# Kernel optimization log

Measured on AMD Instinct MI355X. Metric: run time of the kernel, lower is better.

The kernel has to match this reference:

```python
import jax, jax.numpy as jnp
import numpy as np

CUTOFF = 5.0
NUM_RADIAL = 6
HIDDEN = 128
N_NODES = 100000
N_EDGES = 800000
MAX_Z = 95
P = 6  # envelope_exponent(5) + 1, per PyG Envelope


def _envelope(x):
    # PyG DimeNet Envelope: (1/x + a*x^(p-1) + b*x^p + c*x^(p+1)) * (x < 1)
    a = -(P + 1) * (P + 2) / 2.0   # -28
    b = P * (P + 2)                # 48
    c = -P * (P + 1) / 2.0         # -21
    xp0 = x ** (P - 1)
    xp1 = xp0 * x
    xp2 = xp1 * x
    return (1.0 / x + a * xp0 + b * xp1 + c * xp2) * (x < 1.0)


def setup_inputs():
    key = jax.random.key(0)
    ks = jax.random.split(key, 8)
    z = jax.random.randint(ks[0], (N_NODES,), 0, MAX_Z, dtype=jnp.int32)
    pos = jax.random.normal(ks[1], (N_NODES, 3), dtype=jnp.float32)
    ei = jax.random.randint(ks[2], (2, N_EDGES), 0, N_NODES, dtype=jnp.int32)
    i, j = ei[0], ei[1]
    j = jnp.where(j == i, (j + 1) % N_NODES, j)  # radius_graph emits no self-loops (avoids d=0)
    edge_index = jnp.stack([i, j])
    # BesselBasisLayer learnable frequencies: pi * n
    freq = np.pi * jnp.arange(1, NUM_RADIAL + 1, dtype=jnp.float32)
    s3 = float(np.sqrt(3.0))
    emb_table = jax.random.uniform(ks[3], (MAX_Z, HIDDEN), jnp.float32, -s3, s3)
    W_rbf = jax.random.normal(ks[4], (NUM_RADIAL, HIDDEN), jnp.float32) * (1.0 / np.sqrt(NUM_RADIAL))
    b_rbf = jnp.zeros((HIDDEN,), jnp.float32)
    W_lin = jax.random.normal(ks[5], (3 * HIDDEN, HIDDEN), jnp.float32) * (1.0 / np.sqrt(3 * HIDDEN))
    b_lin = jnp.zeros((HIDDEN,), jnp.float32)
    return {"z": z, "pos": pos, "edge_index": edge_index, "freq": freq,
            "emb_table": emb_table, "W_rbf": W_rbf, "b_rbf": b_rbf,
            "W_lin": W_lin, "b_lin": b_lin}


def reference(z, pos, edge_index, freq, emb_table, W_rbf, b_rbf, W_lin, b_lin):
    n = z.shape[0]
    i, j = edge_index[0], edge_index[1]
    # per-edge distance  [E]
    d = jnp.sqrt(jnp.sum((pos[i] - pos[j]) ** 2, axis=-1))
    # Bessel RBF  [E, num_radial]
    x = d[:, None] / CUTOFF
    rbf = _envelope(x) * jnp.sin(freq * x)
    # DimeNet EmbeddingBlock (act = SiLU/swish)
    h_rbf = jax.nn.silu(rbf @ W_rbf + b_rbf)            # [E, H]
    xz = emb_table[z]                                    # [N, H]
    e_emb = jax.nn.silu(
        jnp.concatenate([xz[i], xz[j], h_rbf], axis=-1) @ W_lin + b_lin
    )                                                    # [E, H]
    # scatter_mean over target node j -> [N, H]
    sums = jax.ops.segment_sum(e_emb, j, num_segments=n)
    cnt = jax.ops.segment_sum(jnp.ones_like(d), j, num_segments=n)
    v_emb = sums / jnp.maximum(cnt, 1.0)[:, None]
    return v_emb  # pool=None -> node-level embeddings
```

## Files before the change

### kernel.cpp

```cpp
#include <hip/hip_runtime.h>
#include <hip/hip_bf16.h>
#include <math.h>

#define HID 128
#define NRAD 6
#define TABN 4096
#define CUTOFF_INV 0.2f
#define MZ 95
#define MZP (MZ + 1)
#define SENT ((MZ << 13) | (MZ << 20))
#define PAD 32
#define OVF_CAP 65536
#define FTR 8

typedef unsigned int uint32;

__global__ void build1(const float* __restrict__ emb, const float* __restrict__ W_lin,
                       const float* __restrict__ freq, const float* __restrict__ W_rbf,
                       const float* __restrict__ b_rbf, const float* __restrict__ b_lin,
                       const int* __restrict__ ei, const float* __restrict__ pos,
                       const int* __restrict__ z,
                       __hip_bfloat16* __restrict__ Tb, float* __restrict__ ftab,
                       int* __restrict__ cnt, int* __restrict__ payload,
                       int* __restrict__ ovfcnt, int2* __restrict__ ovfbuf,
                       int MAXZ, int E) {
    __shared__ float sh[FTR * HID];
    int h   = threadIdx.x;
    int bid = blockIdx.x;
    int nT  = 2 * (MAXZ + 1);
    int nF  = (TABN + FTR) / FTR;
    if (bid < nT) {
        int zz = bid >> 1, s = bid & 1;
        if (zz == MAXZ) {
            Tb[(size_t)(s * (MAXZ + 1) + zz) * HID + h] = __float2bfloat16(-60.0f);
            return;
        }
        sh[h] = emb[zz * HID + h];
        __syncthreads();
        const float* W = W_lin + (size_t)s * HID * HID;
        float acc = (s == 0) ? b_lin[h] : 0.f;
#pragma unroll 8
        for (int k = 0; k < HID; ++k) acc = fmaf(sh[k], W[k * HID + h], acc);
        Tb[(size_t)(s * (MAXZ + 1) + zz) * HID + h] = __float2bfloat16(acc);
    } else if (bid < nT + nF) {
        int t0 = (bid - nT) * FTR;
        for (int r = 0; r < FTR; ++r) {
            int t = t0 + r;
            float rbf[NRAD];
            if (t == 0) {
#pragma unroll
                for (int k = 0; k < NRAD; ++k) rbf[k] = freq[k];
            } else if (t >= TABN) {
#pragma unroll
                for (int k = 0; k < NRAD; ++k) rbf[k] = 0.f;
            } else {
                float x  = (float)t / (float)TABN;
                float x2 = x * x, x5 = x2 * x2 * x;
                float env = 1.f / x + x5 * (-28.f + x * (48.f + x * (-21.f)));
#pragma unroll
                for (int k = 0; k < NRAD; ++k) rbf[k] = env * sinf(freq[k] * x);
            }
            float pre = b_rbf[h];
#pragma unroll
            for (int k = 0; k < NRAD; ++k) pre = fmaf(rbf[k], W_rbf[k * HID + h], pre);
            sh[r * HID + h] = pre / (1.f + __expf(-pre));
        }
        __syncthreads();
        const float* W3 = W_lin + (size_t)2 * HID * HID;
        float acc[FTR];
#pragma unroll
        for (int r = 0; r < FTR; ++r) acc[r] = 0.f;
#pragma unroll 4
        for (int k = 0; k < HID; ++k) {
            float w = W3[k * HID + h];
#pragma unroll
            for (int r = 0; r < FTR; ++r) acc[r] = fmaf(sh[r * HID + k], w, acc[r]);
        }
        for (int r = 0; r < FTR; ++r) {
            int t = t0 + r;
            if (t <= TABN) ftab[(size_t)t * HID + h] = acc[r];
        }
    } else {
        int e = (bid - nT - nF) * HID + h;
        if (e < E) {
            int i = ei[e];
            int j = ei[E + e];
            float dx = pos[3 * i]     - pos[3 * j];
            float dy = pos[3 * i + 1] - pos[3 * j + 1];
            float dz = pos[3 * i + 2] - pos[3 * j + 2];
            float d  = sqrtf(dx * dx + dy * dy + dz * dz);
            float u  = fminf(d * CUTOFF_INV, 1.0f) * (float)TABN;
            int   ti = (int)(u + 0.5f);
            if (ti > TABN) ti = TABN;
            int pl = ti | (z[i] << 13) | (z[j] << 20);
            int r  = atomicAdd(&cnt[j], 1);
            if (r < PAD) {
                payload[(size_t)j * PAD + r] = pl;
            } else {
                int o = atomicAdd(ovfcnt, 1);
                if (o < OVF_CAP) ovfbuf[o] = make_int2(j, pl);
            }
        }
    }
}

#define EDGE_ACC(pl_) do {                                                                    \
    int ti_ = (pl_) & 0x1FFF;                                                                 \
    int zi_ = ((pl_) >> 13) & 0x7F;                                                           \
    int zj_ = ((pl_) >> 20) & 0x7F;                                                           \
    float4 f_ = *(const float4*)((const char*)ftab + (uint32)((ti_ << 9) + fb4));             \
    uint32 a0_ = sT[zi_ * (HID / 2) + l2];                                                    \
    uint32 a1_ = sT[zi_ * (HID / 2) + l2 + 1];                                                \
    uint32 b0_ = sT[(MZP + zj_) * (HID / 2) + l2];                                            \
    uint32 b1_ = sT[(MZP + zj_) * (HID / 2) + l2 + 1];                                        \
    float p0_ = __uint_as_float(a0_ << 16)         + __uint_as_float(b0_ << 16)         + f_.x; \
    float p1_ = __uint_as_float(a0_ & 0xFFFF0000u) + __uint_as_float(b0_ & 0xFFFF0000u) + f_.y; \
    float p2_ = __uint_as_float(a1_ << 16)         + __uint_as_float(b1_ << 16)         + f_.z; \
    float p3_ = __uint_as_float(a1_ & 0xFFFF0000u) + __uint_as_float(b1_ & 0xFFFF0000u) + f_.w; \
    ax = fmaf(p0_, __builtin_amdgcn_rcpf(1.f + __expf(-p0_)), ax);                            \
    ay = fmaf(p1_, __builtin_amdgcn_rcpf(1.f + __expf(-p1_)), ay);                            \
    az = fmaf(p2_, __builtin_amdgcn_rcpf(1.f + __expf(-p2_)), az);                            \
    aw = fmaf(p3_, __builtin_amdgcn_rcpf(1.f + __expf(-p3_)), aw);                            \
} while (0)

__launch_bounds__(1024)
__global__ void gather_k(const int* __restrict__ cnt, const int* __restrict__ payload,
                         const uint32* __restrict__ Tb32, const float* __restrict__ ftab,
                         const int* __restrict__ ovfcnt, const int2* __restrict__ ovfbuf,
                         float* __restrict__ out, int N) {
    __shared__ uint32 sT[2 * MZP * (HID / 2)];
    int tid = threadIdx.x;
    for (int k = tid; k < 2 * MZP * (HID / 2); k += 1024) sT[k] = Tb32[k];
    __syncthreads();

    int lane = tid & 63, wv = tid >> 6;
    int hi   = lane >> 5;
    int l32  = lane & 31;
    int h4   = l32 * 4;
    int l2   = l32 * 2;
    uint32 fb4 = (uint32)h4 << 2;
    int nov  = *ovfcnt;
    if (nov > OVF_CAP) nov = OVF_CAP;
    int nW = gridDim.x << 4;

    for (int n = (blockIdx.x << 4) + wv; n < N; n += nW) {
        int deg = cnt[n];
        int plv = payload[(size_t)n * PAD + l32];
        int cb  = deg < PAD ? deg : PAD;
        plv = (l32 < cb) ? plv : SENT;
        int nit = (cb + 1) >> 1;

        float ax = 0.f, ay = 0.f, az = 0.f, aw = 0.f;
        for (int k = 0; k < nit; ++k) {
            int plA = __builtin_amdgcn_readlane(plv, 2 * k);
            int plB = __builtin_amdgcn_readlane(plv, 2 * k + 1);
            int pl  = hi ? plB : plA;
            EDGE_ACC(pl);
        }
        if (deg > PAD && nov > 0) {
            for (int o = 0; o < nov; ++o) {
                int2 v = ovfbuf[o];
                if (v.x == n) { int pl = v.y; EDGE_ACC(pl); }
            }
        }
        ax += __shfl_xor(ax, 32);
        ay += __shfl_xor(ay, 32);
        az += __shfl_xor(az, 32);
        aw += __shfl_xor(aw, 32);
        if (hi == 0) {
            float s = (deg > 0) ? 1.0f / (float)deg : 0.0f;
            float4 o4;
            o4.x = ax * s; o4.y = ay * s; o4.z = az * s; o4.w = aw * s;
            *(float4*)(out + (size_t)n * HID + h4) = o4;
        }
    }
}

extern "C" void kernel_launch(void* const* d_in, const int* in_sizes, int n_in,
                              void* d_out, int out_size, void* d_ws, size_t ws_size,
                              hipStream_t stream) {
    const int*   z     = (const int*)d_in[0];
    const float* pos   = (const float*)d_in[1];
    const int*   ei    = (const int*)d_in[2];
    const float* freq  = (const float*)d_in[3];
    const float* emb   = (const float*)d_in[4];
    const float* W_rbf = (const float*)d_in[5];
    const float* b_rbf = (const float*)d_in[6];
    const float* W_lin = (const float*)d_in[7];
    const float* b_lin = (const float*)d_in[8];

    int N    = in_sizes[0];
    int E    = in_sizes[2] / 2;
    int MAXZ = in_sizes[4] / HID;
    float* out = (float*)d_out;

    int N_pad = ((N + 1024) / 1024) * 1024;

    char* ws = (char*)d_ws;
    size_t off = 0;
    auto alloc = [&](size_t bytes) { char* p = ws + off; off = (off + bytes + 255) & ~(size_t)255; return p; };
    int*   cnt     = (int*)alloc((size_t)N_pad * 4);
    int*   ovfcnt  = (int*)alloc(256);
    __hip_bfloat16* Tb = (__hip_bfloat16*)alloc((size_t)2 * (MAXZ + 1) * HID * 2);
    float* ftab    = (float*)alloc((size_t)(TABN + 1) * HID * 4);
    int*   payload = (int*)alloc((size_t)N_pad * PAD * 4);
    int2*  ovfbuf  = (int2*)alloc((size_t)OVF_CAP * 8);

    hipMemsetAsync(cnt, 0, (size_t)N_pad * 4 + 256, stream);

    int nBuild = 2 * (MAXZ + 1) + (TABN + FTR) / FTR + (E + HID - 1) / HID;
    build1<<<nBuild, HID, 0, stream>>>(emb, W_lin, freq, W_rbf, b_rbf, b_lin,
                                       ei, pos, z, Tb, ftab, cnt, payload,
                                       ovfcnt, ovfbuf, MAXZ, E);
    gather_k<<<512, 1024, 0, stream>>>(cnt, payload, (const uint32*)Tb, ftab,
                                       ovfcnt, ovfbuf, out, N);
}
```

Baseline: 186.8 us.

## Software-pipeline gather loop, prefetch next node, and fold log2e into tables

The gather loop is software-pipelined: the ftab float4 load for the edge two ahead and the LDS table loads for the next edge are issued before the current edge's compute. Node degree and payload for the next node are prefetched across iterations. The tables are prescaled by log2(e) so the SiLU uses a raw v_exp_f32 with a negated operand, and the result is rescaled by ln2 at output. The sentinel value changes to keep the padded-edge contribution near zero in the new scaling. LDS reads are also widened to uint2. This adds register pressure and relies on the wrapped readlane index hitting sentinel lanes for the tail.

Result: no change. 188.3 us (+0.8%).

```diff
diff --git a/kernel.cpp b/kernel.cpp
--- a/kernel.cpp
+++ b/kernel.cpp
@@ -12,6 +12,8 @@
 #define PAD 32
 #define OVF_CAP 65536
 #define FTR 8
+#define LOG2E 1.4426950408889634f
+#define LN2   0.6931471805599453f
 
 typedef unsigned int uint32;
 
@@ -32,7 +34,7 @@
     if (bid < nT) {
         int zz = bid >> 1, s = bid & 1;
         if (zz == MAXZ) {
-            Tb[(size_t)(s * (MAXZ + 1) + zz) * HID + h] = __float2bfloat16(-60.0f);
+            Tb[(size_t)(s * (MAXZ + 1) + zz) * HID + h] = __float2bfloat16(-86.5f);
             return;
         }
         sh[h] = emb[zz * HID + h];
@@ -41,7 +43,7 @@
         float acc = (s == 0) ? b_lin[h] : 0.f;
 #pragma unroll 8
         for (int k = 0; k < HID; ++k) acc = fmaf(sh[k], W[k * HID + h], acc);
-        Tb[(size_t)(s * (MAXZ + 1) + zz) * HID + h] = __float2bfloat16(acc);
+        Tb[(size_t)(s * (MAXZ + 1) + zz) * HID + h] = __float2bfloat16(acc * LOG2E);
     } else if (bid < nT + nF) {
         int t0 = (bid - nT) * FTR;
         for (int r = 0; r < FTR; ++r) {
@@ -78,7 +80,7 @@
         }
         for (int r = 0; r < FTR; ++r) {
             int t = t0 + r;
-            if (t <= TABN) ftab[(size_t)t * HID + h] = acc[r];
+            if (t <= TABN) ftab[(size_t)t * HID + h] = acc[r] * LOG2E;
         }
     } else {
         int e = (bid - nT - nF) * HID + h;
@@ -104,23 +106,31 @@
     }
 }
 
-#define EDGE_ACC(pl_) do {                                                                    \
-    int ti_ = (pl_) & 0x1FFF;                                                                 \
-    int zi_ = ((pl_) >> 13) & 0x7F;                                                           \
-    int zj_ = ((pl_) >> 20) & 0x7F;                                                           \
-    float4 f_ = *(const float4*)((const char*)ftab + (uint32)((ti_ << 9) + fb4));             \
-    uint32 a0_ = sT[zi_ * (HID / 2) + l2];                                                    \
-    uint32 a1_ = sT[zi_ * (HID / 2) + l2 + 1];                                                \
-    uint32 b0_ = sT[(MZP + zj_) * (HID / 2) + l2];                                            \
-    uint32 b1_ = sT[(MZP + zj_) * (HID / 2) + l2 + 1];                                        \
-    float p0_ = __uint_as_float(a0_ << 16)         + __uint_as_float(b0_ << 16)         + f_.x; \
-    float p1_ = __uint_as_float(a0_ & 0xFFFF0000u) + __uint_as_float(b0_ & 0xFFFF0000u) + f_.y; \
-    float p2_ = __uint_as_float(a1_ << 16)         + __uint_as_float(b1_ << 16)         + f_.z; \
-    float p3_ = __uint_as_float(a1_ & 0xFFFF0000u) + __uint_as_float(b1_ & 0xFFFF0000u) + f_.w; \
-    ax = fmaf(p0_, __builtin_amdgcn_rcpf(1.f + __expf(-p0_)), ax);                            \
-    ay = fmaf(p1_, __builtin_amdgcn_rcpf(1.f + __expf(-p1_)), ay);                            \
-    az = fmaf(p2_, __builtin_amdgcn_rcpf(1.f + __expf(-p2_)), az);                            \
-    aw = fmaf(p3_, __builtin_amdgcn_rcpf(1.f + __expf(-p3_)), aw);                            \
+__device__ __forceinline__ float exp2neg(float x) {
+    float r; asm("v_exp_f32 %0, -%1" : "=v"(r) : "v"(x)); return r;
+}
+
+#define PLSEL(pv_, idx_) (hi ? __builtin_amdgcn_readlane((pv_), 2 * (idx_) + 1) \
+                             : __builtin_amdgcn_readlane((pv_), 2 * (idx_)))
+
+#define FLOAD(pl_) (*(const float4*)((const char*)ftab + (uint32)((((pl_) & 0x1FFF) << 9) + fb4)))
+
+#define TL(pl_, ua_, ub_) do {                                                 \
+    int zi_ = ((pl_) >> 13) & 0x7F;                                            \
+    int zj_ = ((pl_) >> 20) & 0x7F;                                            \
+    ua_ = *(const uint2*)&sT[zi_ * (HID / 2) + l2];                            \
+    ub_ = *(const uint2*)&sT[(MZP + zj_) * (HID / 2) + l2];                    \
+} while (0)
+
+#define COMPUTE(f_, ua_, ub_) do {                                                                 \
+    float p0_ = __uint_as_float(ua_.x << 16)         + __uint_as_float(ub_.x << 16)         + f_.x; \
+    float p1_ = __uint_as_float(ua_.x & 0xFFFF0000u) + __uint_as_float(ub_.x & 0xFFFF0000u) + f_.y; \
+    float p2_ = __uint_as_float(ua_.y << 16)         + __uint_as_float(ub_.y << 16)         + f_.z; \
+    float p3_ = __uint_as_float(ua_.y & 0xFFFF0000u) + __uint_as_float(ub_.y & 0xFFFF0000u) + f_.w; \
+    ax = fmaf(p0_, __builtin_amdgcn_rcpf(1.f + exp2neg(p0_)), ax);                                 \
+    ay = fmaf(p1_, __builtin_amdgcn_rcpf(1.f + exp2neg(p1_)), ay);                                 \
+    az = fmaf(p2_, __builtin_amdgcn_rcpf(1.f + exp2neg(p2_)), az);                                 \
+    aw = fmaf(p3_, __builtin_amdgcn_rcpf(1.f + exp2neg(p3_)), aw);                                 \
 } while (0)
 
 __launch_bounds__(1024)
@@ -138,29 +148,53 @@
     int l32  = lane & 31;
     int h4   = l32 * 4;
     int l2   = l32 * 2;
-    uint32 fb4 = (uint32)h4 << 2;
+    uint32 fb4 = (uint32)l32 << 4;
     int nov  = *ovfcnt;
     if (nov > OVF_CAP) nov = OVF_CAP;
     int nW = gridDim.x << 4;
 
-    for (int n = (blockIdx.x << 4) + wv; n < N; n += nW) {
-        int deg = cnt[n];
-        int plv = payload[(size_t)n * PAD + l32];
+    int n = (blockIdx.x << 4) + wv;
+    int degC = 0, plvC = SENT;
+    if (n < N) { degC = cnt[n]; plvC = payload[(size_t)n * PAD + l32]; }
+
+    while (n < N) {
+        int n2 = n + nW;
+        int degN = 0, plvN = SENT;
+        if (n2 < N) { degN = cnt[n2]; plvN = payload[(size_t)n2 * PAD + l32]; }
+
+        int deg = degC;
         int cb  = deg < PAD ? deg : PAD;
-        plv = (l32 < cb) ? plv : SENT;
+        int plv = (l32 < cb) ? plvC : SENT;
         int nit = (cb + 1) >> 1;
 
         float ax = 0.f, ay = 0.f, az = 0.f, aw = 0.f;
-        for (int k = 0; k < nit; ++k) {
-            int plA = __builtin_amdgcn_readlane(plv, 2 * k);
-            int plB = __builtin_amdgcn_readlane(plv, 2 * k + 1);
-            int pl  = hi ? plB : plA;
-            EDGE_ACC(pl);
+        if (nit > 0) {
+            int pl0 = PLSEL(plv, 0);
+            float4 f0 = FLOAD(pl0);
+            uint2 ua, ub; TL(pl0, ua, ub);
+            int plL = PLSEL(plv, 1);
+            float4 f1 = FLOAD(plL);
+#pragma unroll 2
+            for (int k = 0; k < nit; ++k) {
+                int kk  = (k + 2) & 15;
+                int pl2 = PLSEL(plv, kk);
+                float4 f2 = FLOAD(pl2);
+                uint2 va, vb; TL(plL, va, vb);
+                COMPUTE(f0, ua, ub);
+                f0 = f1; f1 = f2;
+                ua = va; ub = vb;
+                plL = pl2;
+            }
         }
         if (deg > PAD && nov > 0) {
             for (int o = 0; o < nov; ++o) {
                 int2 v = ovfbuf[o];
-                if (v.x == n) { int pl = v.y; EDGE_ACC(pl); }
+                if (v.x == n) {
+                    int pl = v.y;
+                    float4 f_ = FLOAD(pl);
+                    uint2 ua_, ub_; TL(pl, ua_, ub_);
+                    COMPUTE(f_, ua_, ub_);
+                }
             }
         }
         ax += __shfl_xor(ax, 32);
@@ -168,11 +202,12 @@
         az += __shfl_xor(az, 32);
         aw += __shfl_xor(aw, 32);
         if (hi == 0) {
-            float s = (deg > 0) ? 1.0f / (float)deg : 0.0f;
+            float s = (deg > 0) ? LN2 / (float)deg : 0.0f;
             float4 o4;
             o4.x = ax * s; o4.y = ay * s; o4.z = az * s; o4.w = aw * s;
             *(float4*)(out + (size_t)n * HID + h4) = o4;
         }
+        n = n2; degC = degN; plvC = plvN;
     }
 }
 
```
